# Optimization experiments

Measured on AMD Instinct MI355X. Metric: run time of the kernel, lower is better.

Reference implementation:

```python
import jax, jax.numpy as jnp
import numpy as np

HEADS = 4

def setup_inputs() -> dict:
    B, L, D = 4, 2048, 256
    key = jax.random.key(0)
    k1, k2, k3, k4, k5, k6 = jax.random.split(key, 6)
    return {
        "atten": jax.random.normal(k1, (B, L, L), dtype=jnp.float32),
        "value": jax.random.normal(k2, (B, L, D), dtype=jnp.float32),
        "mask": jax.random.uniform(k3, (B, 1, L, L), dtype=jnp.float32),
        "padding_mask": jax.random.randint(k4, (B, L, L), 0, 2, dtype=jnp.int32),
        "Wv": jax.random.normal(k5, (D, D), dtype=jnp.float32) * 0.02,
        "bv": jnp.zeros((D,), dtype=jnp.float32),
        "Wo": jax.random.normal(k6, (D, D), dtype=jnp.float32) * 0.02,
        "bo": jnp.zeros((D,), dtype=jnp.float32),
    }

def reference(atten, value, mask, padding_mask, Wv, bv, Wo, bo):
    B, L, D = value.shape
    H = HEADS
    dk = D // H
    # to_value: Linear then split heads. N == 1 (value.unsqueeze(1) in torch).
    v = value @ Wv + bv                                   # (B, L, D)
    v = v.reshape(B, 1, L, H, dk).transpose(0, 3, 1, 2, 4)  # (B, H, N=1, L, dk)
    # externally supplied attention logits, two sequential masked fills
    a = atten[:, None, :, :]                              # (B, 1, L, L)
    a = jnp.where(mask < 0.5, jnp.finfo(a.dtype).min, a)
    a = jnp.where(padding_mask[:, None, :, :] == 0, -jnp.inf, a)
    a = jax.nn.softmax(a, axis=-1)                        # (B, 1, L, L)
    # dropout is identity in eval mode
    # einsum 'bhij,bhnjk->bhnik' with h=1 on a broadcast across H heads of v
    out = jnp.einsum('bij,bhnjk->bhnik', a[:, 0], v)      # (B, H, 1, L, dk)
    out = out.transpose(0, 2, 3, 1, 4).reshape(B, 1, L, D)
    out = out @ Wo + bo                                   # (B, 1, L, D)
    return out
```

## Files before the change

kernel.cpp:

```cpp
#include <hip/hip_runtime.h>
#include <hip/hip_bf16.h>
#include <math.h>

#define L 2048
#define D 256
#define NEG_FLT_MAX (-3.402823466e38f)

typedef __attribute__((ext_vector_type(8))) short bf16x8;
typedef __attribute__((ext_vector_type(4))) float f32x4;
typedef __attribute__((ext_vector_type(4))) int i32x4;

__device__ __forceinline__ unsigned short f2bf(float f) {
    union { float f; unsigned int u; } v; v.f = f;
    unsigned int r = v.u + 0x7FFFu + ((v.u >> 16) & 1u);
    return (unsigned short)(r >> 16);
}

__global__ __launch_bounds__(256) void wtrans_kernel(
    const float* __restrict__ Wv, const float* __restrict__ Wo,
    unsigned short* __restrict__ Wvt, unsigned short* __restrict__ Wot) {
    int idx = blockIdx.x * 256 + threadIdx.x;
    int which = idx >> 16;
    int e = idx & 65535;
    int n = e >> 8, k = e & 255;
    const float* W = which ? Wo : Wv;
    unsigned short* Wt = which ? Wot : Wvt;
    Wt[n * 256 + k] = f2bf(W[k * 256 + n]);
}

template<int MODE>
__global__ __launch_bounds__(256) void gemm_kernel(
    const float* __restrict__ A,
    const unsigned short* __restrict__ Wt,
    const float* __restrict__ bias,
    unsigned short* __restrict__ Vt,
    float* __restrict__ Cout) {
    const int wave = threadIdx.x >> 6;
    const int lane = threadIdx.x & 63;
    const int mh = wave >> 1, nh = wave & 1;
    const int lm = lane & 15, q = lane >> 4;
    const int m0 = blockIdx.x * 64;
    const int n0 = blockIdx.y * 128;

    f32x4 acc[2][4];
#pragma unroll
    for (int i = 0; i < 2; i++)
#pragma unroll
        for (int j = 0; j < 4; j++) acc[i][j] = (f32x4)(0.f);

    int arow[2];
    arow[0] = m0 + mh * 32 + lm;
    arow[1] = arow[0] + 16;
    int ncol[4];
#pragma unroll
    for (int nf = 0; nf < 4; nf++) ncol[nf] = n0 + nh * 64 + nf * 16 + lm;

    for (int k0 = 0; k0 < 256; k0 += 32) {
        int kq = k0 + q * 8;
        bf16x8 bfr[4];
#pragma unroll
        for (int nf = 0; nf < 4; nf++)
            bfr[nf] = *reinterpret_cast<const bf16x8*>(Wt + ncol[nf] * 256 + kq);
        bf16x8 afr[2];
#pragma unroll
        for (int mf = 0; mf < 2; mf++) {
            const float* ap = A + arow[mf] * 256 + kq;
            f32x4 a0 = *reinterpret_cast<const f32x4*>(ap);
            f32x4 a1 = *reinterpret_cast<const f32x4*>(ap + 4);
            bf16x8 t;
#pragma unroll
            for (int e = 0; e < 4; e++) t[e] = (short)f2bf(a0[e]);
#pragma unroll
            for (int e = 0; e < 4; e++) t[4 + e] = (short)f2bf(a1[e]);
            afr[mf] = t;
        }
#pragma unroll
        for (int mf = 0; mf < 2; mf++)
#pragma unroll
            for (int nf = 0; nf < 4; nf++)
                acc[mf][nf] = __builtin_amdgcn_mfma_f32_16x16x32_bf16(
                    afr[mf], bfr[nf], acc[mf][nf], 0, 0, 0);
    }

#pragma unroll
    for (int mf = 0; mf < 2; mf++) {
        int mrow = m0 + mh * 32 + mf * 16 + q * 4;
#pragma unroll
        for (int nf = 0; nf < 4; nf++) {
            int n = ncol[nf];
            float bias_n = bias[n];
            if (MODE == 0) {
                int b = mrow >> 11;
                int j = mrow & 2047;
                unsigned short* dst = Vt + (size_t)b * (D * L) + (size_t)n * L + j;
                ushort4 pk;
                pk.x = f2bf(acc[mf][nf][0] + bias_n);
                pk.y = f2bf(acc[mf][nf][1] + bias_n);
                pk.z = f2bf(acc[mf][nf][2] + bias_n);
                pk.w = f2bf(acc[mf][nf][3] + bias_n);
                *reinterpret_cast<ushort4*>(dst) = pk;
            } else {
#pragma unroll
                for (int r = 0; r < 4; r++)
                    Cout[(size_t)(mrow + r) * 256 + n] = acc[mf][nf][r] + bias_n;
            }
        }
    }
}

__global__ __launch_bounds__(256) void attn_kernel(
    const float* __restrict__ atten, const float* __restrict__ mask,
    const int* __restrict__ pad, const unsigned short* __restrict__ Vt,
    float* __restrict__ part) {
    const int blk = blockIdx.x;
    const int rb = blk >> 1, js = blk & 1;
    const int b = rb >> 6;
    const int i0 = (rb & 63) * 32;
    const int tid = threadIdx.x;
    const int wave = tid >> 6, lane = tid & 63;
    const int lm = lane & 15, q = lane >> 4;
    const int r = tid >> 3;
    const int c0 = (tid & 7) * 8;

    __shared__ __align__(16) unsigned short Plds[2][32][72];
    __shared__ float alpha_lds[2][32];

    f32x4 acc[2][4];
#pragma unroll
    for (int i = 0; i < 2; i++)
#pragma unroll
        for (int j = 0; j < 4; j++) acc[i][j] = (f32x4)(0.f);

    float m_run = -INFINITY, l_run = 0.f;

    const size_t rowoff = ((size_t)(b * L + i0 + r)) * L + js * 1024 + c0;
    const float* at_row = atten + rowoff;
    const float* mk_row = mask + rowoff;
    const int* pd_row = pad + rowoff;
    const unsigned short* vt_b = Vt + (size_t)b * (D * L) + js * 1024;

    for (int jt = 0; jt < 16; jt++) {
        const int j0 = jt * 64;
        bf16x8 bfr[2][4];
#pragma unroll
        for (int kk = 0; kk < 2; kk++)
#pragma unroll
            for (int nf = 0; nf < 4; nf++) {
                int n = wave * 64 + nf * 16 + lm;
                bfr[kk][nf] = *reinterpret_cast<const bf16x8*>(
                    vt_b + (size_t)n * L + j0 + kk * 32 + q * 8);
            }
        f32x4 a0 = *reinterpret_cast<const f32x4*>(at_row + j0);
        f32x4 a1 = *reinterpret_cast<const f32x4*>(at_row + j0 + 4);
        f32x4 k0 = *reinterpret_cast<const f32x4*>(mk_row + j0);
        f32x4 k1 = *reinterpret_cast<const f32x4*>(mk_row + j0 + 4);
        i32x4 p0 = *reinterpret_cast<const i32x4*>(pd_row + j0);
        i32x4 p1 = *reinterpret_cast<const i32x4*>(pd_row + j0 + 4);
        float s[8];
#pragma unroll
        for (int e = 0; e < 4; e++) {
            float sv = (k0[e] < 0.5f) ? NEG_FLT_MAX : a0[e];
            s[e] = (p0[e] == 0) ? -INFINITY : sv;
            float sw = (k1[e] < 0.5f) ? NEG_FLT_MAX : a1[e];
            s[4 + e] = (p1[e] == 0) ? -INFINITY : sw;
        }
        float tmax = s[0];
#pragma unroll
        for (int e = 1; e < 8; e++) tmax = fmaxf(tmax, s[e]);
#pragma unroll
        for (int off = 1; off < 8; off <<= 1) tmax = fmaxf(tmax, __shfl_xor(tmax, off));
        float m_new = fmaxf(m_run, tmax);
        bool inf_row = (m_new == -INFINITY);
        float alpha = inf_row ? 1.f : __expf(m_run - m_new);
        float psum = 0.f;
        bf16x8 pk;
#pragma unroll
        for (int e = 0; e < 8; e++) {
            float pv = inf_row ? 0.f : __expf(s[e] - m_new);
            psum += pv;
            pk[e] = (short)f2bf(pv);
        }
#pragma unroll
        for (int off = 1; off < 8; off <<= 1) psum += __shfl_xor(psum, off);
        l_run = l_run * alpha + psum;
        m_run = m_new;

        const int par = jt & 1;
        *reinterpret_cast<bf16x8*>(&Plds[par][r][c0]) = pk;
        if ((tid & 7) == 0) alpha_lds[par][r] = alpha;
        __syncthreads();

        float al[2][4];
#pragma unroll
        for (int mf = 0; mf < 2; mf++)
#pragma unroll
            for (int rg = 0; rg < 4; rg++) al[mf][rg] = alpha_lds[par][mf * 16 + q * 4 + rg];
#pragma unroll
        for (int mf = 0; mf < 2; mf++)
#pragma unroll
            for (int nf = 0; nf < 4; nf++)
#pragma unroll
                for (int rg = 0; rg < 4; rg++) acc[mf][nf][rg] *= al[mf][rg];

#pragma unroll
        for (int kk = 0; kk < 2; kk++)
#pragma unroll
            for (int mf = 0; mf < 2; mf++) {
                bf16x8 afr = *reinterpret_cast<const bf16x8*>(
                    &Plds[par][mf * 16 + lm][kk * 32 + q * 8]);
#pragma unroll
                for (int nf = 0; nf < 4; nf++)
                    acc[mf][nf] = __builtin_amdgcn_mfma_f32_16x16x32_bf16(
                        afr, bfr[kk][nf], acc[mf][nf], 0, 0, 0);
            }
    }

    float* pbase = part + (size_t)blk * 8256;
#pragma unroll
    for (int mf = 0; mf < 2; mf++)
#pragma unroll
        for (int nf = 0; nf < 4; nf++) {
            int n = wave * 64 + nf * 16 + lm;
#pragma unroll
            for (int rg = 0; rg < 4; rg++)
                pbase[(mf * 16 + q * 4 + rg) * 256 + n] = acc[mf][nf][rg];
        }
    if ((tid & 7) == 0) {
        pbase[8192 + r] = m_run;
        pbase[8224 + r] = l_run;
    }
}

__global__ __launch_bounds__(256) void combine_kernel(
    const float* __restrict__ part, float* __restrict__ out1) {
    const int rb = blockIdx.x;
    const int t = threadIdx.x;
    const int r = t >> 3;
    const int n0 = (t & 7) * 32;
    const float* p0 = part + (size_t)(rb * 2) * 8256;
    const float* p1 = p0 + 8256;
    float m0 = p0[8192 + r], l0 = p0[8224 + r];
    float m1 = p1[8192 + r], l1 = p1[8224 + r];
    float M = fmaxf(m0, m1);
    float w0 = (m0 == -INFINITY) ? 0.f : __expf(m0 - M);
    float w1 = (m1 == -INFINITY) ? 0.f : __expf(m1 - M);
    float inv = 1.f / (l0 * w0 + l1 * w1);
    w0 *= inv; w1 *= inv;
    float* dst = out1 + ((size_t)rb * 32 + r) * 256 + n0;
    const float* a0 = p0 + r * 256 + n0;
    const float* a1 = p1 + r * 256 + n0;
#pragma unroll
    for (int e = 0; e < 32; e += 4) {
        f32x4 x0 = *reinterpret_cast<const f32x4*>(a0 + e);
        f32x4 x1 = *reinterpret_cast<const f32x4*>(a1 + e);
        f32x4 o = x0 * w0 + x1 * w1;
        *reinterpret_cast<f32x4*>(dst + e) = o;
    }
}

extern "C" void kernel_launch(void* const* d_in, const int* in_sizes, int n_in,
                              void* d_out, int out_size, void* d_ws, size_t ws_size,
                              hipStream_t stream) {
    (void)in_sizes; (void)n_in; (void)out_size; (void)ws_size;
    const float* atten = (const float*)d_in[0];
    const float* value = (const float*)d_in[1];
    const float* mask  = (const float*)d_in[2];
    const int*   pad   = (const int*)d_in[3];
    const float* Wv    = (const float*)d_in[4];
    const float* bv    = (const float*)d_in[5];
    const float* Wo    = (const float*)d_in[6];
    const float* bo    = (const float*)d_in[7];
    float* out = (float*)d_out;

    char* ws = (char*)d_ws;
    unsigned short* Vt  = (unsigned short*)(ws);
    unsigned short* Wvt = (unsigned short*)(ws + 4194304);
    unsigned short* Wot = (unsigned short*)(ws + 4325376);
    float* out1 = (float*)(ws + 4456448);
    float* part = (float*)(ws + 12845056);

    wtrans_kernel<<<512, 256, 0, stream>>>(Wv, Wo, Wvt, Wot);
    gemm_kernel<0><<<dim3(128, 2), 256, 0, stream>>>(value, Wvt, bv, Vt, nullptr);
    attn_kernel<<<512, 256, 0, stream>>>(atten, mask, pad, Vt, part);
    combine_kernel<<<256, 256, 0, stream>>>(part, out1);
    gemm_kernel<1><<<dim3(128, 2), 256, 0, stream>>>(out1, Wot, bo, nullptr, out);
}
```

Before: 251.1 us.

## Fuse split-K combine into output GEMM, widen attention split and prefetch inputs

Splits the attention key dimension four ways instead of two, doubling the block count to raise occupancy while streaming the large atten/mask/padding tensors. Adds a one-step register prefetch of the next tile's mask and logit loads. Removes the separate combine kernel and the out1 buffer by merging the four partials with their softmax rescaling directly inside the output projection GEMM's A-operand load. Both GEMMs are retiled to 64x64 per block with one 16-row strip per wave. The output GEMM now rereads four partial buffers per n-tile, and the attention pass writes more partial data.

```diff
diff --git a/kernel.cpp b/kernel.cpp
--- a/kernel.cpp
+++ b/kernel.cpp
@@ -28,32 +28,25 @@
     Wt[n * 256 + k] = f2bf(W[k * 256 + n]);
 }
 
-template<int MODE>
-__global__ __launch_bounds__(256) void gemm_kernel(
+__global__ __launch_bounds__(256) void gemm_v_kernel(
     const float* __restrict__ A,
     const unsigned short* __restrict__ Wt,
     const float* __restrict__ bias,
-    unsigned short* __restrict__ Vt,
-    float* __restrict__ Cout) {
+    unsigned short* __restrict__ Vt) {
     const int wave = threadIdx.x >> 6;
     const int lane = threadIdx.x & 63;
-    const int mh = wave >> 1, nh = wave & 1;
     const int lm = lane & 15, q = lane >> 4;
     const int m0 = blockIdx.x * 64;
-    const int n0 = blockIdx.y * 128;
-
-    f32x4 acc[2][4];
-#pragma unroll
-    for (int i = 0; i < 2; i++)
-#pragma unroll
-        for (int j = 0; j < 4; j++) acc[i][j] = (f32x4)(0.f);
-
-    int arow[2];
-    arow[0] = m0 + mh * 32 + lm;
-    arow[1] = arow[0] + 16;
+    const int n0 = blockIdx.y * 64;
+    const int arow = m0 + wave * 16 + lm;
+
     int ncol[4];
 #pragma unroll
-    for (int nf = 0; nf < 4; nf++) ncol[nf] = n0 + nh * 64 + nf * 16 + lm;
+    for (int nf = 0; nf < 4; nf++) ncol[nf] = n0 + nf * 16 + lm;
+
+    f32x4 acc[4];
+#pragma unroll
+    for (int nf = 0; nf < 4; nf++) acc[nf] = (f32x4)(0.f);
 
     for (int k0 = 0; k0 < 256; k0 += 32) {
         int kq = k0 + q * 8;
@@ -61,59 +54,43 @@
 #pragma unroll
         for (int nf = 0; nf < 4; nf++)
             bfr[nf] = *reinterpret_cast<const bf16x8*>(Wt + ncol[nf] * 256 + kq);
-        bf16x8 afr[2];
-#pragma unroll
-        for (int mf = 0; mf < 2; mf++) {
-            const float* ap = A + arow[mf] * 256 + kq;
-            f32x4 a0 = *reinterpret_cast<const f32x4*>(ap);
-            f32x4 a1 = *reinterpret_cast<const f32x4*>(ap + 4);
-            bf16x8 t;
-#pragma unroll
-            for (int e = 0; e < 4; e++) t[e] = (short)f2bf(a0[e]);
-#pragma unroll
-            for (int e = 0; e < 4; e++) t[4 + e] = (short)f2bf(a1[e]);
-            afr[mf] = t;
-        }
-#pragma unroll
-        for (int mf = 0; mf < 2; mf++)
-#pragma unroll
-            for (int nf = 0; nf < 4; nf++)
-                acc[mf][nf] = __builtin_amdgcn_mfma_f32_16x16x32_bf16(
-                    afr[mf], bfr[nf], acc[mf][nf], 0, 0, 0);
-    }
-
-#pragma unroll
-    for (int mf = 0; mf < 2; mf++) {
-        int mrow = m0 + mh * 32 + mf * 16 + q * 4;
-#pragma unroll
-        for (int nf = 0; nf < 4; nf++) {
-            int n = ncol[nf];
-            float bias_n = bias[n];
-            if (MODE == 0) {
-                int b = mrow >> 11;
-                int j = mrow & 2047;
-                unsigned short* dst = Vt + (size_t)b * (D * L) + (size_t)n * L + j;
-                ushort4 pk;
-                pk.x = f2bf(acc[mf][nf][0] + bias_n);
-                pk.y = f2bf(acc[mf][nf][1] + bias_n);
-                pk.z = f2bf(acc[mf][nf][2] + bias_n);
-                pk.w = f2bf(acc[mf][nf][3] + bias_n);
-                *reinterpret_cast<ushort4*>(dst) = pk;
-            } else {
-#pragma unroll
-                for (int r = 0; r < 4; r++)
-                    Cout[(size_t)(mrow + r) * 256 + n] = acc[mf][nf][r] + bias_n;
-            }
-        }
-    }
-}
-
-__global__ __launch_bounds__(256) void attn_kernel(
+        const float* ap = A + (size_t)arow * 256 + kq;
+        f32x4 a0 = *reinterpret_cast<const f32x4*>(ap);
+        f32x4 a1 = *reinterpret_cast<const f32x4*>(ap + 4);
+        bf16x8 afr;
+#pragma unroll
+        for (int e = 0; e < 4; e++) afr[e] = (short)f2bf(a0[e]);
+#pragma unroll
+        for (int e = 0; e < 4; e++) afr[4 + e] = (short)f2bf(a1[e]);
+#pragma unroll
+        for (int nf = 0; nf < 4; nf++)
+            acc[nf] = __builtin_amdgcn_mfma_f32_16x16x32_bf16(
+                afr, bfr[nf], acc[nf], 0, 0, 0);
+    }
+
+    int mrow = m0 + wave * 16 + q * 4;
+    int b = mrow >> 11;
+    int j = mrow & 2047;
+#pragma unroll
+    for (int nf = 0; nf < 4; nf++) {
+        int n = ncol[nf];
+        float bias_n = bias[n];
+        unsigned short* dst = Vt + (size_t)b * (D * L) + (size_t)n * L + j;
+        ushort4 pk;
+        pk.x = f2bf(acc[nf][0] + bias_n);
+        pk.y = f2bf(acc[nf][1] + bias_n);
+        pk.z = f2bf(acc[nf][2] + bias_n);
+        pk.w = f2bf(acc[nf][3] + bias_n);
+        *reinterpret_cast<ushort4*>(dst) = pk;
+    }
+}
+
+__global__ __launch_bounds__(256, 4) void attn_kernel(
     const float* __restrict__ atten, const float* __restrict__ mask,
     const int* __restrict__ pad, const unsigned short* __restrict__ Vt,
     float* __restrict__ part) {
     const int blk = blockIdx.x;
-    const int rb = blk >> 1, js = blk & 1;
+    const int rb = blk >> 2, js = blk & 3;
     const int b = rb >> 6;
     const int i0 = (rb & 63) * 32;
     const int tid = threadIdx.x;
@@ -133,13 +110,20 @@
 
     float m_run = -INFINITY, l_run = 0.f;
 
-    const size_t rowoff = ((size_t)(b * L + i0 + r)) * L + js * 1024 + c0;
+    const size_t rowoff = ((size_t)(b * L + i0 + r)) * L + js * 512 + c0;
     const float* at_row = atten + rowoff;
     const float* mk_row = mask + rowoff;
     const int* pd_row = pad + rowoff;
-    const unsigned short* vt_b = Vt + (size_t)b * (D * L) + js * 1024;
-
-    for (int jt = 0; jt < 16; jt++) {
+    const unsigned short* vt_b = Vt + (size_t)b * (D * L) + js * 512;
+
+    f32x4 na0 = *reinterpret_cast<const f32x4*>(at_row);
+    f32x4 na1 = *reinterpret_cast<const f32x4*>(at_row + 4);
+    f32x4 nk0 = *reinterpret_cast<const f32x4*>(mk_row);
+    f32x4 nk1 = *reinterpret_cast<const f32x4*>(mk_row + 4);
+    i32x4 np0 = *reinterpret_cast<const i32x4*>(pd_row);
+    i32x4 np1 = *reinterpret_cast<const i32x4*>(pd_row + 4);
+
+    for (int jt = 0; jt < 8; jt++) {
         const int j0 = jt * 64;
         bf16x8 bfr[2][4];
 #pragma unroll
@@ -150,12 +134,16 @@
                 bfr[kk][nf] = *reinterpret_cast<const bf16x8*>(
                     vt_b + (size_t)n * L + j0 + kk * 32 + q * 8);
             }
-        f32x4 a0 = *reinterpret_cast<const f32x4*>(at_row + j0);
-        f32x4 a1 = *reinterpret_cast<const f32x4*>(at_row + j0 + 4);
-        f32x4 k0 = *reinterpret_cast<const f32x4*>(mk_row + j0);
-        f32x4 k1 = *reinterpret_cast<const f32x4*>(mk_row + j0 + 4);
-        i32x4 p0 = *reinterpret_cast<const i32x4*>(pd_row + j0);
-        i32x4 p1 = *reinterpret_cast<const i32x4*>(pd_row + j0 + 4);
+        f32x4 a0 = na0, a1 = na1, k0 = nk0, k1 = nk1;
+        i32x4 p0 = np0, p1 = np1;
+        if (jt < 7) {
+            na0 = *reinterpret_cast<const f32x4*>(at_row + j0 + 64);
+            na1 = *reinterpret_cast<const f32x4*>(at_row + j0 + 68);
+            nk0 = *reinterpret_cast<const f32x4*>(mk_row + j0 + 64);
+            nk1 = *reinterpret_cast<const f32x4*>(mk_row + j0 + 68);
+            np0 = *reinterpret_cast<const i32x4*>(pd_row + j0 + 64);
+            np1 = *reinterpret_cast<const i32x4*>(pd_row + j0 + 68);
+        }
         float s[8];
 #pragma unroll
         for (int e = 0; e < 4; e++) {
@@ -231,30 +219,78 @@
     }
 }
 
-__global__ __launch_bounds__(256) void combine_kernel(
-    const float* __restrict__ part, float* __restrict__ out1) {
-    const int rb = blockIdx.x;
-    const int t = threadIdx.x;
-    const int r = t >> 3;
-    const int n0 = (t & 7) * 32;
-    const float* p0 = part + (size_t)(rb * 2) * 8256;
-    const float* p1 = p0 + 8256;
-    float m0 = p0[8192 + r], l0 = p0[8224 + r];
-    float m1 = p1[8192 + r], l1 = p1[8224 + r];
-    float M = fmaxf(m0, m1);
-    float w0 = (m0 == -INFINITY) ? 0.f : __expf(m0 - M);
-    float w1 = (m1 == -INFINITY) ? 0.f : __expf(m1 - M);
-    float inv = 1.f / (l0 * w0 + l1 * w1);
-    w0 *= inv; w1 *= inv;
-    float* dst = out1 + ((size_t)rb * 32 + r) * 256 + n0;
-    const float* a0 = p0 + r * 256 + n0;
-    const float* a1 = p1 + r * 256 + n0;
-#pragma unroll
-    for (int e = 0; e < 32; e += 4) {
-        f32x4 x0 = *reinterpret_cast<const f32x4*>(a0 + e);
-        f32x4 x1 = *reinterpret_cast<const f32x4*>(a1 + e);
-        f32x4 o = x0 * w0 + x1 * w1;
-        *reinterpret_cast<f32x4*>(dst + e) = o;
+__global__ __launch_bounds__(256) void gemm_out_kernel(
+    const float* __restrict__ part,
+    const unsigned short* __restrict__ Wt,
+    const float* __restrict__ bias,
+    float* __restrict__ Cout) {
+    const int wave = threadIdx.x >> 6;
+    const int lane = threadIdx.x & 63;
+    const int lm = lane & 15, q = lane >> 4;
+    const int m0 = blockIdx.x * 64;
+    const int n0 = blockIdx.y * 64;
+    const int arow = m0 + wave * 16 + lm;
+    const int rb = arow >> 5, r_in = arow & 31;
+    const float* pb = part + (size_t)rb * 4 * 8256;
+
+    float w[4], lj[4];
+    float M = -INFINITY;
+#pragma unroll
+    for (int js = 0; js < 4; js++) {
+        w[js] = pb[(size_t)js * 8256 + 8192 + r_in];
+        lj[js] = pb[(size_t)js * 8256 + 8224 + r_in];
+        M = fmaxf(M, w[js]);
+    }
+    float lsum = 0.f;
+#pragma unroll
+    for (int js = 0; js < 4; js++) {
+        w[js] = (w[js] == -INFINITY) ? 0.f : __expf(w[js] - M);
+        lsum += lj[js] * w[js];
+    }
+    float inv = 1.f / lsum;
+#pragma unroll
+    for (int js = 0; js < 4; js++) w[js] *= inv;
+
+    int ncol[4];
+#pragma unroll
+    for (int nf = 0; nf < 4; nf++) ncol[nf] = n0 + nf * 16 + lm;
+
+    f32x4 acc[4];
+#pragma unroll
+    for (int nf = 0; nf < 4; nf++) acc[nf] = (f32x4)(0.f);
+
+    for (int k0 = 0; k0 < 256; k0 += 32) {
+        int kq = k0 + q * 8;
+        bf16x8 bfr[4];
+#pragma unroll
+        for (int nf = 0; nf < 4; nf++)
+            bfr[nf] = *reinterpret_cast<const bf16x8*>(Wt + ncol[nf] * 256 + kq);
+        f32x4 s0 = (f32x4)(0.f), s1 = (f32x4)(0.f);
+#pragma unroll
+        for (int js = 0; js < 4; js++) {
+            const float* ap = pb + (size_t)js * 8256 + r_in * 256 + kq;
+            s0 += *reinterpret_cast<const f32x4*>(ap) * w[js];
+            s1 += *reinterpret_cast<const f32x4*>(ap + 4) * w[js];
+        }
+        bf16x8 afr;
+#pragma unroll
+        for (int e = 0; e < 4; e++) afr[e] = (short)f2bf(s0[e]);
+#pragma unroll
+        for (int e = 0; e < 4; e++) afr[4 + e] = (short)f2bf(s1[e]);
+#pragma unroll
+        for (int nf = 0; nf < 4; nf++)
+            acc[nf] = __builtin_amdgcn_mfma_f32_16x16x32_bf16(
+                afr, bfr[nf], acc[nf], 0, 0, 0);
+    }
+
+    int mrow = m0 + wave * 16 + q * 4;
+#pragma unroll
+    for (int nf = 0; nf < 4; nf++) {
+        int n = ncol[nf];
+        float bias_n = bias[n];
+#pragma unroll
+        for (int rg = 0; rg < 4; rg++)
+            Cout[(size_t)(mrow + rg) * 256 + n] = acc[nf][rg] + bias_n;
     }
 }
 
@@ -276,12 +312,10 @@
     unsigned short* Vt  = (unsigned short*)(ws);
     unsigned short* Wvt = (unsigned short*)(ws + 4194304);
     unsigned short* Wot = (unsigned short*)(ws + 4325376);
-    float* out1 = (float*)(ws + 4456448);
-    float* part = (float*)(ws + 12845056);
+    float* part = (float*)(ws + 4456448);
 
     wtrans_kernel<<<512, 256, 0, stream>>>(Wv, Wo, Wvt, Wot);
-    gemm_kernel<0><<<dim3(128, 2), 256, 0, stream>>>(value, Wvt, bv, Vt, nullptr);
-    attn_kernel<<<512, 256, 0, stream>>>(atten, mask, pad, Vt, part);
-    combine_kernel<<<256, 256, 0, stream>>>(part, out1);
-    gemm_kernel<1><<<dim3(128, 2), 256, 0, stream>>>(out1, Wot, bo, nullptr, out);
-}
+    gemm_v_kernel<<<dim3(128, 4), 256, 0, stream>>>(value, Wvt, bv, Vt);
+    attn_kernel<<<1024, 256, 0, stream>>>(atten, mask, pad, Vt, part);
+    gemm_out_kernel<<<dim3(128, 4), 256, 0, stream>>>(part, Wot, bo, out);
+}
```

After: 274.8 us. 9.5% more time.
